# Performance work log

Measured on AMD Instinct MI355X. Metric: run time of the kernel, lower is better.

The kernel has to match this reference:

```python
import jax, jax.numpy as jnp
import numpy as np

N, K, F = 262144, 256, 128
LAMB = 1.0
EPS = 1e-16


def setup_inputs() -> dict:
    key = jax.random.key(0)
    kx, = jax.random.split(key, 1)
    x = jax.random.normal(kx, (N, F), dtype=jnp.float32)
    # Faithful SVD-orthonormal init of cluster centers (num_clusters > feature_size branch)
    rng = np.random.RandomState(0)
    m_np = rng.rand(K, F)
    m_np = m_np.T                      # (F, K) since K > F
    _, _, vh = np.linalg.svd(m_np, full_matrices=False)  # vh: (F, K)
    m_np = vh[:K].T                    # (K, F), orthonormal columns
    m = jnp.asarray(m_np, dtype=jnp.float32)
    s1 = jnp.ones((K,), dtype=jnp.float32)
    s2 = jnp.ones((K,), dtype=jnp.float32)
    return {"x": x, "m": m, "s1": s1, "s2": s2}


def _p_all(x, m, s):
    # x: (N,F), m: (K,F), s: (K,) -> p: (N,K)
    # squared distances via gram expansion (single GEMM instead of per-sample loop)
    d2 = (jnp.sum(x * x, axis=1, keepdims=True)
          + jnp.sum(m * m, axis=1)[None, :]
          - 2.0 * (x @ m.T))
    d2 = jnp.maximum(d2, 0.0)
    logits = -d2 / (s * s)[None, :]
    return jax.nn.softmax(logits, axis=-1)


def _entropy(p):
    # shannon entropy with the original's clamping of p into (0,1)
    p = jnp.clip(p, EPS, 1.0 - EPS)
    return -jnp.sum(p * jnp.log(p), axis=-1)


def reference(x, m, s1, s2):
    # F.normalize(x): L2-normalize rows with eps=1e-12
    xn = x / jnp.maximum(jnp.linalg.norm(x, axis=1, keepdims=True), 1e-12)
    p = _p_all(xn, m, s1)              # (N,K)
    intra = jnp.mean(_entropy(p))      # scalar
    # inter: entropy of the assignment of the mean center against all centers
    xm = jnp.mean(m, axis=0)           # (F,)
    d = jnp.linalg.norm(xm[None, :] - m, axis=1)  # (K,)
    pi = jax.nn.softmax(-((d / s2) ** 2))
    inter = _entropy(pi)
    total = intra - LAMB * inter
    return (total, intra, inter)
```

## Files before the change

kernel.cpp:

```cpp
#include <hip/hip_runtime.h>
#include <hip/hip_bf16.h>


#define N_ROWS 262144

typedef __attribute__((ext_vector_type(8))) short bf16x8;
typedef __attribute__((ext_vector_type(4))) float f32x4;
typedef __attribute__((ext_vector_type(4))) unsigned short u16x4;

__device__ __forceinline__ unsigned short bf16_rne(float x) {
    unsigned int u = __float_as_uint(x);
    u += 0x7FFFu + ((u >> 16) & 1u);
    return (unsigned short)(u >> 16);
}
__device__ __forceinline__ float bf16f(unsigned short h) {
    return __uint_as_float(((unsigned int)h) << 16);
}

__global__ __launch_bounds__(256) void prep(
    const float* __restrict__ m, const float* __restrict__ s1,
    unsigned short* __restrict__ mhi_g, float* __restrict__ mn2_g,
    float* __restrict__ invs_g)
{
    const int t    = threadIdx.x;
    const int lane = t & 63;
    const int k    = blockIdx.x * 8 + (t >> 5);
    const int f4   = t & 31;
    float4 v = reinterpret_cast<const float4*>(m)[k * 32 + f4];
    float pn = v.x*v.x + v.y*v.y + v.z*v.z + v.w*v.w;
    #pragma unroll
    for (int msk = 1; msk <= 16; msk <<= 1) pn += __shfl_xor(pn, msk);
    if ((lane & 31) == 0) {
        mn2_g[k] = pn;
        float sv = s1[k];
        invs_g[k] = 1.0f / (sv * sv);
    }
    const int f0 = f4 << 2;
    const int c = k >> 4, n = k & 15, s = f0 >> 5, blk = (f0 >> 3) & 3, i0 = f0 & 7;
    const int elem = ((c * 4 + s) * 64 + blk * 16 + n) * 8 + i0;
    float xs[4] = {v.x, v.y, v.z, v.w};
    u16x4 hh;
    #pragma unroll
    for (int q = 0; q < 4; ++q) hh[q] = bf16_rne(xs[q]);
    *(u16x4*)(mhi_g + elem) = hh;
}

__global__ __launch_bounds__(256, 1) void fused_main(
    const float* __restrict__ x, const unsigned short* __restrict__ mhi_g,
    const float* __restrict__ mn2_g, const float* __restrict__ invs_g,
    float* __restrict__ wavesum)
{
    const int tid  = threadIdx.x;
    const int lane = tid & 63;
    const int w    = tid >> 6;
    const int rw   = lane & 15;
    const int blkl = lane >> 4;
    const int gw   = blockIdx.x * 4 + w;

    bf16x8 B[64];
    #pragma unroll
    for (int j = 0; j < 64; ++j)
        B[j] = *(const bf16x8*)(mhi_g + (j * 64 + lane) * 8);

    float bkv[16], isv[16];
    #pragma unroll
    for (int c = 0; c < 16; ++c) {
        bkv[c] = 1.0f + mn2_g[c * 16 + rw];
        isv[c] = invs_g[c * 16 + rw];
    }

    const float* xbase = x + (size_t)(gw * 256 + rw) * 128 + blkl * 8;

    float4 px[8];
    #pragma unroll
    for (int s = 0; s < 4; ++s) {
        px[2*s]   = *(const float4*)(xbase + s * 32);
        px[2*s+1] = *(const float4*)(xbase + s * 32 + 4);
    }

    float ent = 0.0f;

    for (int t = 0; t < 16; ++t) {
        bf16x8 ah[4], al[4];
        float n2 = 0.0f;
        #pragma unroll
        for (int s = 0; s < 4; ++s) {
            float xs[8] = {px[2*s].x, px[2*s].y, px[2*s].z, px[2*s].w,
                           px[2*s+1].x, px[2*s+1].y, px[2*s+1].z, px[2*s+1].w};
            #pragma unroll
            for (int q = 0; q < 8; ++q) {
                n2 += xs[q] * xs[q];
                unsigned short h = bf16_rne(xs[q]);
                float r = xs[q] - bf16f(h);
                ah[s][q] = (short)h;
                al[s][q] = (short)bf16_rne(r);
            }
        }
        if (t != 15) {
            const float* p = xbase + (size_t)(t + 1) * 16 * 128;
            #pragma unroll
            for (int s = 0; s < 4; ++s) {
                px[2*s]   = *(const float4*)(p + s * 32);
                px[2*s+1] = *(const float4*)(p + s * 32 + 4);
            }
        }
        f32x4 acc[16];
        #pragma unroll
        for (int c = 0; c < 16; ++c) acc[c] = f32x4{0.f, 0.f, 0.f, 0.f};
        #pragma unroll
        for (int s = 0; s < 4; ++s) {
            #pragma unroll
            for (int c = 0; c < 16; ++c) {
                acc[c] = __builtin_amdgcn_mfma_f32_16x16x32_bf16(al[s], B[c*4+s], acc[c], 0, 0, 0);
                acc[c] = __builtin_amdgcn_mfma_f32_16x16x32_bf16(ah[s], B[c*4+s], acc[c], 0, 0, 0);
            }
        }
        n2 += __shfl_xor(n2, 16);
        n2 += __shfl_xor(n2, 32);
        float a2 = 2.0f / fmaxf(sqrtf(n2), 1e-12f);
        #pragma unroll
        for (int reg = 0; reg < 4; ++reg) {
            float ar = __shfl(a2, blkl * 4 + reg);
            float S = 0.f, T = 0.f;
            #pragma unroll
            for (int c = 0; c < 16; ++c) {
                float l = fminf(ar * acc[c][reg] - bkv[c], 0.0f) * isv[c];
                float e = __expf(l);
                S += e;
                T += l * e;
            }
            #pragma unroll
            for (int msk = 1; msk <= 8; msk <<= 1) {
                S += __shfl_xor(S, msk);
                T += __shfl_xor(T, msk);
            }
            if (rw == 0) ent += __logf(S) - T / S;
        }
    }

    ent += __shfl_xor(ent, 16);
    ent += __shfl_xor(ent, 32);
    if (lane == 0) wavesum[gw] = ent;
}

__global__ __launch_bounds__(1024) void finalize(
    const float* __restrict__ wavesum, const float* __restrict__ m,
    const float* __restrict__ s2, float* __restrict__ out)
{
    __shared__ float xmp[8][128];
    __shared__ float xm[128];
    __shared__ double dred[16];
    __shared__ float redS[16], redT[16];
    const int tid  = threadIdx.x;
    const int lane = tid & 63;
    const int w    = tid >> 6;

    double ds = (double)wavesum[tid];
    #pragma unroll
    for (int msk = 1; msk <= 32; msk <<= 1) ds += __shfl_xor(ds, msk);
    if (lane == 0) dred[w] = ds;

    {
        const int f = tid & 127, g = tid >> 7;
        const float* mp = m + (size_t)g * 32 * 128 + f;
        float cs = 0.f;
        #pragma unroll 8
        for (int k = 0; k < 32; ++k) cs += mp[(size_t)k * 128];
        xmp[g][f] = cs;
    }
    __syncthreads();
    if (tid < 128) {
        float s = 0.f;
        #pragma unroll
        for (int g = 0; g < 8; ++g) s += xmp[g][tid];
        xm[tid] = s * (1.0f / 256.0f);
    }
    __syncthreads();

    const int k = tid >> 2, q = tid & 3;
    float d2 = 0.f;
    {
        const float4* mr  = (const float4*)(m + (size_t)k * 128) + q * 8;
        const float4* xv4 = (const float4*)xm + q * 8;
        #pragma unroll
        for (int j = 0; j < 8; ++j) {
            float4 mv = mr[j], xv = xv4[j];
            float dx = xv.x - mv.x, dy = xv.y - mv.y,
                  dz = xv.z - mv.z, dw = xv.w - mv.w;
            d2 += dx*dx + dy*dy + dz*dz + dw*dw;
        }
    }
    d2 += __shfl_xor(d2, 1);
    d2 += __shfl_xor(d2, 2);
    float sv = s2[k];
    float rr = sqrtf(d2) / sv;
    float lg = -(rr * rr);
    float e  = (q == 0) ? __expf(lg) : 0.f;
    float S = e, T = (q == 0) ? lg * e : 0.f;
    #pragma unroll
    for (int msk = 1; msk <= 32; msk <<= 1) {
        S += __shfl_xor(S, msk);
        T += __shfl_xor(T, msk);
    }
    if (lane == 0) { redS[w] = S; redT[w] = T; }
    __syncthreads();
    if (tid == 0) {
        float Sa = 0.f, Ta = 0.f;
        double intra_d = 0.0;
        #pragma unroll
        for (int i = 0; i < 16; ++i) {
            Sa += redS[i]; Ta += redT[i]; intra_d += dred[i];
        }
        float inter = __logf(Sa) - Ta / Sa;
        float intra = (float)(intra_d / (double)N_ROWS);
        out[0] = intra - inter;
        out[1] = intra;
        out[2] = inter;
    }
}

extern "C" void kernel_launch(void* const* d_in, const int* in_sizes, int n_in,
                              void* d_out, int out_size, void* d_ws, size_t ws_size,
                              hipStream_t stream) {
    const float* x  = (const float*)d_in[0];
    const float* m  = (const float*)d_in[1];
    const float* s1 = (const float*)d_in[2];
    const float* s2 = (const float*)d_in[3];
    float* out = (float*)d_out;

    char* ws = (char*)d_ws;
    unsigned short* mhi_g = (unsigned short*)ws;
    float* mn2_g   = (float*)(ws + 65536);
    float* invs_g  = (float*)(ws + 65536 + 1024);
    float* wavesum = (float*)(ws + 65536 + 2048);

    prep<<<dim3(32), dim3(256), 0, stream>>>(m, s1, mhi_g, mn2_g, invs_g);
    fused_main<<<dim3(256), dim3(256), 0, stream>>>(x, mhi_g, mn2_g, invs_g, wavesum);
    finalize<<<dim3(1), dim3(1024), 0, stream>>>(wavesum, m, s2, out);
}
```

Baseline: 249.0 us.

## Split cluster columns across two waves per row tile and reduce softmax partials in LDS

Each 128-thread block now handles 256 rows with two waves, each wave owning half of the 256 cluster columns. This halves the B-fragment registers per wave and allows two blocks per CU. Per-row softmax partial sums (S, T) are combined through shared memory before the entropy is computed, and the grid grows to 1024 blocks. The x loads are split into two halves interleaved with the MFMA steps, and the bf16 hi/lo split uses packed conversion intrinsics. The cost is that each row's x tile is loaded and converted twice (once per wave), plus extra LDS traffic and barriers.

```diff
diff --git a/kernel.cpp b/kernel.cpp
--- a/kernel.cpp
+++ b/kernel.cpp
@@ -7,14 +7,12 @@
 typedef __attribute__((ext_vector_type(8))) short bf16x8;
 typedef __attribute__((ext_vector_type(4))) float f32x4;
 typedef __attribute__((ext_vector_type(4))) unsigned short u16x4;
+typedef __attribute__((ext_vector_type(4))) unsigned int u32x4;
 
 __device__ __forceinline__ unsigned short bf16_rne(float x) {
     unsigned int u = __float_as_uint(x);
     u += 0x7FFFu + ((u >> 16) & 1u);
     return (unsigned short)(u >> 16);
-}
-__device__ __forceinline__ float bf16f(unsigned short h) {
-    return __uint_as_float(((unsigned int)h) << 16);
 }
 
 __global__ __launch_bounds__(256) void prep(
@@ -45,102 +43,153 @@
     *(u16x4*)(mhi_g + elem) = hh;
 }
 
-__global__ __launch_bounds__(256, 1) void fused_main(
+__device__ __forceinline__ void cvt8(float4 a, float4 b, bf16x8& hi, bf16x8& lo,
+                                     float& n2a, float& n2b) {
+    float xs[8] = {a.x, a.y, a.z, a.w, b.x, b.y, b.z, b.w};
+    u32x4 hp, lp;
+    #pragma unroll
+    for (int p = 0; p < 4; ++p) {
+        float e = xs[2*p], o = xs[2*p+1];
+        n2a += e * e;
+        n2b += o * o;
+        __hip_bfloat162 hv = __float22bfloat162_rn(make_float2(e, o));
+        unsigned hu = *reinterpret_cast<unsigned*>(&hv);
+        float ef = __uint_as_float(hu << 16);
+        float of = __uint_as_float(hu & 0xffff0000u);
+        __hip_bfloat162 lv = __float22bfloat162_rn(make_float2(e - ef, o - of));
+        hp[p] = hu;
+        lp[p] = *reinterpret_cast<unsigned*>(&lv);
+    }
+    hi = *reinterpret_cast<bf16x8*>(&hp);
+    lo = *reinterpret_cast<bf16x8*>(&lp);
+}
+
+__global__ __launch_bounds__(128, 2) void fused_main(
     const float* __restrict__ x, const unsigned short* __restrict__ mhi_g,
     const float* __restrict__ mn2_g, const float* __restrict__ invs_g,
     float* __restrict__ wavesum)
 {
+    __shared__ float part[2][16][16][2];
+    __shared__ float redw[2];
+
     const int tid  = threadIdx.x;
     const int lane = tid & 63;
     const int w    = tid >> 6;
     const int rw   = lane & 15;
     const int blkl = lane >> 4;
-    const int gw   = blockIdx.x * 4 + w;
-
-    bf16x8 B[64];
-    #pragma unroll
-    for (int j = 0; j < 64; ++j)
-        B[j] = *(const bf16x8*)(mhi_g + (j * 64 + lane) * 8);
-
-    float bkv[16], isv[16];
-    #pragma unroll
-    for (int c = 0; c < 16; ++c) {
-        bkv[c] = 1.0f + mn2_g[c * 16 + rw];
-        isv[c] = invs_g[c * 16 + rw];
-    }
-
-    const float* xbase = x + (size_t)(gw * 256 + rw) * 128 + blkl * 8;
-
-    float4 px[8];
-    #pragma unroll
-    for (int s = 0; s < 4; ++s) {
-        px[2*s]   = *(const float4*)(xbase + s * 32);
-        px[2*s+1] = *(const float4*)(xbase + s * 32 + 4);
-    }
-
-    float ent = 0.0f;
+
+    bf16x8 B[32];
+    #pragma unroll
+    for (int jc = 0; jc < 8; ++jc)
+        #pragma unroll
+        for (int s = 0; s < 4; ++s)
+            B[jc*4+s] = *(const bf16x8*)(mhi_g + (((8*w + jc)*4 + s)*64 + lane)*8);
+
+    float bkv[8], isv[8];
+    #pragma unroll
+    for (int jc = 0; jc < 8; ++jc) {
+        int col = (8*w + jc)*16 + rw;
+        bkv[jc] = 1.0f + mn2_g[col];
+        isv[jc] = invs_g[col];
+    }
+
+    const float* xb = x + (size_t)(blockIdx.x*256 + rw)*128 + blkl*8;
+
+    float4 pxA[4], pxB[4];
+    #pragma unroll
+    for (int s = 0; s < 2; ++s) {
+        pxA[2*s]   = *(const float4*)(xb + s*32);
+        pxA[2*s+1] = *(const float4*)(xb + s*32 + 4);
+    }
+    #pragma unroll
+    for (int s = 2; s < 4; ++s) {
+        pxB[2*(s-2)]   = *(const float4*)(xb + s*32);
+        pxB[2*(s-2)+1] = *(const float4*)(xb + s*32 + 4);
+    }
+
+    #define MFMA_STEP(s_)                                                        \
+        do { _Pragma("unroll")                                                   \
+            for (int jc = 0; jc < 8; ++jc) {                                     \
+                acc[jc] = __builtin_amdgcn_mfma_f32_16x16x32_bf16(al, B[jc*4+(s_)], acc[jc], 0, 0, 0); \
+                acc[jc] = __builtin_amdgcn_mfma_f32_16x16x32_bf16(ah, B[jc*4+(s_)], acc[jc], 0, 0, 0); \
+            } } while (0)
 
     for (int t = 0; t < 16; ++t) {
-        bf16x8 ah[4], al[4];
-        float n2 = 0.0f;
-        #pragma unroll
-        for (int s = 0; s < 4; ++s) {
-            float xs[8] = {px[2*s].x, px[2*s].y, px[2*s].z, px[2*s].w,
-                           px[2*s+1].x, px[2*s+1].y, px[2*s+1].z, px[2*s+1].w};
-            #pragma unroll
-            for (int q = 0; q < 8; ++q) {
-                n2 += xs[q] * xs[q];
-                unsigned short h = bf16_rne(xs[q]);
-                float r = xs[q] - bf16f(h);
-                ah[s][q] = (short)h;
-                al[s][q] = (short)bf16_rne(r);
-            }
-        }
-        if (t != 15) {
-            const float* p = xbase + (size_t)(t + 1) * 16 * 128;
-            #pragma unroll
-            for (int s = 0; s < 4; ++s) {
-                px[2*s]   = *(const float4*)(p + s * 32);
-                px[2*s+1] = *(const float4*)(p + s * 32 + 4);
-            }
-        }
-        f32x4 acc[16];
-        #pragma unroll
-        for (int c = 0; c < 16; ++c) acc[c] = f32x4{0.f, 0.f, 0.f, 0.f};
-        #pragma unroll
-        for (int s = 0; s < 4; ++s) {
-            #pragma unroll
-            for (int c = 0; c < 16; ++c) {
-                acc[c] = __builtin_amdgcn_mfma_f32_16x16x32_bf16(al[s], B[c*4+s], acc[c], 0, 0, 0);
-                acc[c] = __builtin_amdgcn_mfma_f32_16x16x32_bf16(ah[s], B[c*4+s], acc[c], 0, 0, 0);
-            }
-        }
+        const float* xn = xb + (size_t)(t + 1)*2048;
+        f32x4 acc[8];
+        #pragma unroll
+        for (int jc = 0; jc < 8; ++jc) acc[jc] = f32x4{0.f, 0.f, 0.f, 0.f};
+
+        float n2a = 0.f, n2b = 0.f;
+        bf16x8 ah, al;
+
+        cvt8(pxA[0], pxA[1], ah, al, n2a, n2b);
+        MFMA_STEP(0);
+        cvt8(pxA[2], pxA[3], ah, al, n2a, n2b);
+        MFMA_STEP(1);
+        if (t < 15) {
+            #pragma unroll
+            for (int s = 0; s < 2; ++s) {
+                pxA[2*s]   = *(const float4*)(xn + s*32);
+                pxA[2*s+1] = *(const float4*)(xn + s*32 + 4);
+            }
+        }
+        cvt8(pxB[0], pxB[1], ah, al, n2a, n2b);
+        MFMA_STEP(2);
+        cvt8(pxB[2], pxB[3], ah, al, n2a, n2b);
+        MFMA_STEP(3);
+        if (t < 15) {
+            #pragma unroll
+            for (int s = 2; s < 4; ++s) {
+                pxB[2*(s-2)]   = *(const float4*)(xn + s*32);
+                pxB[2*(s-2)+1] = *(const float4*)(xn + s*32 + 4);
+            }
+        }
+
+        float n2 = n2a + n2b;
         n2 += __shfl_xor(n2, 16);
         n2 += __shfl_xor(n2, 32);
         float a2 = 2.0f / fmaxf(sqrtf(n2), 1e-12f);
         #pragma unroll
         for (int reg = 0; reg < 4; ++reg) {
-            float ar = __shfl(a2, blkl * 4 + reg);
-            float S = 0.f, T = 0.f;
-            #pragma unroll
-            for (int c = 0; c < 16; ++c) {
-                float l = fminf(ar * acc[c][reg] - bkv[c], 0.0f) * isv[c];
+            float ar = __shfl(a2, blkl*4 + reg);
+            float S0 = 0.f, S1 = 0.f, T0 = 0.f, T1 = 0.f;
+            #pragma unroll
+            for (int jc = 0; jc < 8; ++jc) {
+                float l = fminf(ar * acc[jc][reg] - bkv[jc], 0.0f) * isv[jc];
                 float e = __expf(l);
-                S += e;
-                T += l * e;
-            }
+                if (jc & 1) { S1 += e; T1 += l * e; }
+                else        { S0 += e; T0 += l * e; }
+            }
+            float S = S0 + S1, T = T0 + T1;
             #pragma unroll
             for (int msk = 1; msk <= 8; msk <<= 1) {
                 S += __shfl_xor(S, msk);
                 T += __shfl_xor(T, msk);
             }
-            if (rw == 0) ent += __logf(S) - T / S;
-        }
-    }
-
-    ent += __shfl_xor(ent, 16);
-    ent += __shfl_xor(ent, 32);
-    if (lane == 0) wavesum[gw] = ent;
+            if (rw == 0) {
+                float2 st = make_float2(S, T);
+                *(float2*)&part[w][t][blkl*4 + reg][0] = st;
+            }
+        }
+    }
+    #undef MFMA_STEP
+
+    __syncthreads();
+
+    float entloc = 0.f;
+    #pragma unroll
+    for (int r2 = 0; r2 < 2; ++r2) {
+        int r = tid*2 + r2, c = r >> 4, r16 = r & 15;
+        float S = part[0][c][r16][0] + part[1][c][r16][0];
+        float T = part[0][c][r16][1] + part[1][c][r16][1];
+        entloc += __logf(S) - T / S;
+    }
+    #pragma unroll
+    for (int msk = 1; msk <= 32; msk <<= 1) entloc += __shfl_xor(entloc, msk);
+    if (lane == 0) redw[w] = entloc;
+    __syncthreads();
+    if (tid == 0) wavesum[blockIdx.x] = redw[0] + redw[1];
 }
 
 __global__ __launch_bounds__(1024) void finalize(
@@ -235,6 +284,6 @@
     float* wavesum = (float*)(ws + 65536 + 2048);
 
     prep<<<dim3(32), dim3(256), 0, stream>>>(m, s1, mhi_g, mn2_g, invs_g);
-    fused_main<<<dim3(256), dim3(256), 0, stream>>>(x, mhi_g, mn2_g, invs_g, wavesum);
+    fused_main<<<dim3(1024), dim3(128), 0, stream>>>(x, mhi_g, mn2_g, invs_g, wavesum);
     finalize<<<dim3(1), dim3(1024), 0, stream>>>(wavesum, m, s2, out);
 }
```

New measurement: 239.4 us. 3.9% less time.

## Split cluster dimension across waves, shrink register footprint, raise occupancy

Applied to the files above, without the earlier changes.

Work is redistributed so each wave of a block holds only 64 of the 256 cluster columns in registers (16 B fragments instead of 64), and partial softmax sums are combined across waves through shared memory. The grid grows from 256 to 2048 blocks with launch bounds allowing 3 blocks per CU, aiming to hide memory latency through occupancy rather than one block per CU. The 1/s² scale and center norms are folded into the bf16 center matrix and a single per-cluster bias in prep, and x conversion uses packed bf16x2 conversions with a three-slot register prefetch ring. This adds an extra block-level reduction, shared-memory traffic and bf16 rounding of the pre-scaled centers.

```diff
diff --git a/kernel.cpp b/kernel.cpp
--- a/kernel.cpp
+++ b/kernel.cpp
@@ -13,14 +13,31 @@
     u += 0x7FFFu + ((u >> 16) & 1u);
     return (unsigned short)(u >> 16);
 }
-__device__ __forceinline__ float bf16f(unsigned short h) {
-    return __uint_as_float(((unsigned int)h) << 16);
+
+__device__ __forceinline__ void cvt8(float4 a, float4 b, bf16x8& hi, bf16x8& lo,
+                                     float& n2) {
+    float xs[8] = {a.x, a.y, a.z, a.w, b.x, b.y, b.z, b.w};
+    unsigned hp[4], lp[4];
+    #pragma unroll
+    for (int p = 0; p < 4; ++p) {
+        float e = xs[2*p], o = xs[2*p+1];
+        n2 = __builtin_fmaf(e, e, n2);
+        n2 = __builtin_fmaf(o, o, n2);
+        __hip_bfloat162 hv = __float22bfloat162_rn(make_float2(e, o));
+        unsigned hu = *reinterpret_cast<unsigned*>(&hv);
+        float ef = __uint_as_float(hu << 16);
+        float of = __uint_as_float(hu & 0xffff0000u);
+        __hip_bfloat162 lv = __float22bfloat162_rn(make_float2(e - ef, o - of));
+        hp[p] = hu;
+        lp[p] = *reinterpret_cast<unsigned*>(&lv);
+    }
+    hi = *reinterpret_cast<bf16x8*>(hp);
+    lo = *reinterpret_cast<bf16x8*>(lp);
 }
 
 __global__ __launch_bounds__(256) void prep(
     const float* __restrict__ m, const float* __restrict__ s1,
-    unsigned short* __restrict__ mhi_g, float* __restrict__ mn2_g,
-    float* __restrict__ invs_g)
+    unsigned short* __restrict__ mhi_g, float* __restrict__ p2_g)
 {
     const int t    = threadIdx.x;
     const int lane = t & 63;
@@ -30,121 +47,124 @@
     float pn = v.x*v.x + v.y*v.y + v.z*v.z + v.w*v.w;
     #pragma unroll
     for (int msk = 1; msk <= 16; msk <<= 1) pn += __shfl_xor(pn, msk);
-    if ((lane & 31) == 0) {
-        mn2_g[k] = pn;
-        float sv = s1[k];
-        invs_g[k] = 1.0f / (sv * sv);
-    }
+    float sv  = s1[k];
+    float isv = 1.0f / (sv * sv);
+    if ((lane & 31) == 0) p2_g[k] = (1.0f + pn) * isv;
     const int f0 = f4 << 2;
     const int c = k >> 4, n = k & 15, s = f0 >> 5, blk = (f0 >> 3) & 3, i0 = f0 & 7;
     const int elem = ((c * 4 + s) * 64 + blk * 16 + n) * 8 + i0;
-    float xs[4] = {v.x, v.y, v.z, v.w};
+    float xs[4] = {v.x * isv, v.y * isv, v.z * isv, v.w * isv};
     u16x4 hh;
     #pragma unroll
     for (int q = 0; q < 4; ++q) hh[q] = bf16_rne(xs[q]);
     *(u16x4*)(mhi_g + elem) = hh;
 }
 
-__global__ __launch_bounds__(256, 1) void fused_main(
+__global__ __launch_bounds__(256, 3) void fused_main(
     const float* __restrict__ x, const unsigned short* __restrict__ mhi_g,
-    const float* __restrict__ mn2_g, const float* __restrict__ invs_g,
-    float* __restrict__ wavesum)
+    const float* __restrict__ p2_g, float* __restrict__ blocksum)
 {
+    __shared__ float p2s[256];
+    __shared__ float part[8][16][4][2];
+    __shared__ float entred[4];
+
     const int tid  = threadIdx.x;
     const int lane = tid & 63;
     const int w    = tid >> 6;
     const int rw   = lane & 15;
     const int blkl = lane >> 4;
-    const int gw   = blockIdx.x * 4 + w;
-
-    bf16x8 B[64];
-    #pragma unroll
-    for (int j = 0; j < 64; ++j)
-        B[j] = *(const bf16x8*)(mhi_g + (j * 64 + lane) * 8);
-
-    float bkv[16], isv[16];
-    #pragma unroll
-    for (int c = 0; c < 16; ++c) {
-        bkv[c] = 1.0f + mn2_g[c * 16 + rw];
-        isv[c] = invs_g[c * 16 + rw];
-    }
-
-    const float* xbase = x + (size_t)(gw * 256 + rw) * 128 + blkl * 8;
-
-    float4 px[8];
-    #pragma unroll
-    for (int s = 0; s < 4; ++s) {
-        px[2*s]   = *(const float4*)(xbase + s * 32);
-        px[2*s+1] = *(const float4*)(xbase + s * 32 + 4);
-    }
-
-    float ent = 0.0f;
-
-    for (int t = 0; t < 16; ++t) {
-        bf16x8 ah[4], al[4];
-        float n2 = 0.0f;
-        #pragma unroll
-        for (int s = 0; s < 4; ++s) {
-            float xs[8] = {px[2*s].x, px[2*s].y, px[2*s].z, px[2*s].w,
-                           px[2*s+1].x, px[2*s+1].y, px[2*s+1].z, px[2*s+1].w};
+
+    p2s[tid] = p2_g[tid];
+
+    bf16x8 MB[16];
+    #pragma unroll
+    for (int tt = 0; tt < 4; ++tt)
+        #pragma unroll
+        for (int s = 0; s < 4; ++s)
+            MB[tt*4+s] = *(const bf16x8*)(mhi_g + (((4*w + tt)*4 + s)*64 + lane)*8);
+
+    __syncthreads();
+
+    const float* xb = x + (size_t)(blockIdx.x * 128 + rw) * 128 + blkl * 8;
+
+    float4 PA[3], PB[3];
+    #pragma unroll
+    for (int g = 0; g < 3; ++g) {
+        PA[g] = *(const float4*)(xb + g * 32);
+        PB[g] = *(const float4*)(xb + g * 32 + 4);
+    }
+
+    f32x4 acc[4];
+    float n2 = 0.0f;
+
+    #pragma unroll
+    for (int g = 0; g < 32; ++g) {
+        const int s = g & 3;
+        const int slot = g % 3;
+        if (s == 0) {
             #pragma unroll
-            for (int q = 0; q < 8; ++q) {
-                n2 += xs[q] * xs[q];
-                unsigned short h = bf16_rne(xs[q]);
-                float r = xs[q] - bf16f(h);
-                ah[s][q] = (short)h;
-                al[s][q] = (short)bf16_rne(r);
-            }
-        }
-        if (t != 15) {
-            const float* p = xbase + (size_t)(t + 1) * 16 * 128;
-            #pragma unroll
-            for (int s = 0; s < 4; ++s) {
-                px[2*s]   = *(const float4*)(p + s * 32);
-                px[2*s+1] = *(const float4*)(p + s * 32 + 4);
-            }
-        }
-        f32x4 acc[16];
-        #pragma unroll
-        for (int c = 0; c < 16; ++c) acc[c] = f32x4{0.f, 0.f, 0.f, 0.f};
-        #pragma unroll
-        for (int s = 0; s < 4; ++s) {
-            #pragma unroll
-            for (int c = 0; c < 16; ++c) {
-                acc[c] = __builtin_amdgcn_mfma_f32_16x16x32_bf16(al[s], B[c*4+s], acc[c], 0, 0, 0);
-                acc[c] = __builtin_amdgcn_mfma_f32_16x16x32_bf16(ah[s], B[c*4+s], acc[c], 0, 0, 0);
-            }
-        }
-        n2 += __shfl_xor(n2, 16);
-        n2 += __shfl_xor(n2, 32);
-        float a2 = 2.0f / fmaxf(sqrtf(n2), 1e-12f);
-        #pragma unroll
-        for (int reg = 0; reg < 4; ++reg) {
-            float ar = __shfl(a2, blkl * 4 + reg);
+            for (int tt = 0; tt < 4; ++tt) acc[tt] = f32x4{0.f, 0.f, 0.f, 0.f};
+            n2 = 0.0f;
+        }
+        bf16x8 ah, al;
+        cvt8(PA[slot], PB[slot], ah, al, n2);
+        if (g + 3 < 32) {
+            const int g2 = g + 3;
+            const float* p = xb + (size_t)(g2 >> 2) * 2048 + (g2 & 3) * 32;
+            PA[slot] = *(const float4*)(p);
+            PB[slot] = *(const float4*)(p + 4);
+        }
+        #pragma unroll
+        for (int tt = 0; tt < 4; ++tt) {
+            acc[tt] = __builtin_amdgcn_mfma_f32_16x16x32_bf16(MB[tt*4+s], al, acc[tt], 0, 0, 0);
+            acc[tt] = __builtin_amdgcn_mfma_f32_16x16x32_bf16(MB[tt*4+s], ah, acc[tt], 0, 0, 0);
+        }
+        if (s == 3) {
+            const int t = g >> 2;
+            float nn = n2;
+            nn += __shfl_xor(nn, 16);
+            nn += __shfl_xor(nn, 32);
+            float ar = 2.0f / fmaxf(sqrtf(nn), 1e-12f);
             float S = 0.f, T = 0.f;
             #pragma unroll
-            for (int c = 0; c < 16; ++c) {
-                float l = fminf(ar * acc[c][reg] - bkv[c], 0.0f) * isv[c];
-                float e = __expf(l);
-                S += e;
-                T += l * e;
+            for (int tt = 0; tt < 4; ++tt) {
+                f32x4 p2v = *(const f32x4*)&p2s[(4*w + tt)*16 + blkl*4];
+                #pragma unroll
+                for (int r = 0; r < 4; ++r) {
+                    float l = fminf(__builtin_fmaf(ar, acc[tt][r], -p2v[r]), 0.0f);
+                    float e = __expf(l);
+                    S += e;
+                    T = __builtin_fmaf(l, e, T);
+                }
             }
-            #pragma unroll
-            for (int msk = 1; msk <= 8; msk <<= 1) {
-                S += __shfl_xor(S, msk);
-                T += __shfl_xor(T, msk);
-            }
-            if (rw == 0) ent += __logf(S) - T / S;
-        }
-    }
-
-    ent += __shfl_xor(ent, 16);
-    ent += __shfl_xor(ent, 32);
-    if (lane == 0) wavesum[gw] = ent;
+            S += __shfl_xor(S, 16);  T += __shfl_xor(T, 16);
+            S += __shfl_xor(S, 32);  T += __shfl_xor(T, 32);
+            if (blkl == 0)
+                *(float2*)&part[t][rw][w][0] = make_float2(S, T);
+        }
+    }
+
+    __syncthreads();
+
+    float entl = 0.0f;
+    if (tid < 128) {
+        const int c = tid >> 4, r16 = tid & 15;
+        float S = part[c][r16][0][0] + part[c][r16][1][0]
+                + part[c][r16][2][0] + part[c][r16][3][0];
+        float T = part[c][r16][0][1] + part[c][r16][1][1]
+                + part[c][r16][2][1] + part[c][r16][3][1];
+        entl = __logf(S) - T / S;
+    }
+    #pragma unroll
+    for (int msk = 1; msk <= 32; msk <<= 1) entl += __shfl_xor(entl, msk);
+    if (lane == 0) entred[w] = entl;
+    __syncthreads();
+    if (tid == 0)
+        blocksum[blockIdx.x] = entred[0] + entred[1] + entred[2] + entred[3];
 }
 
 __global__ __launch_bounds__(1024) void finalize(
-    const float* __restrict__ wavesum, const float* __restrict__ m,
+    const float* __restrict__ blocksum, const float* __restrict__ m,
     const float* __restrict__ s2, float* __restrict__ out)
 {
     __shared__ float xmp[8][128];
@@ -155,7 +175,7 @@
     const int lane = tid & 63;
     const int w    = tid >> 6;
 
-    double ds = (double)wavesum[tid];
+    double ds = (double)blocksum[tid] + (double)blocksum[tid + 1024];
     #pragma unroll
     for (int msk = 1; msk <= 32; msk <<= 1) ds += __shfl_xor(ds, msk);
     if (lane == 0) dred[w] = ds;
@@ -230,11 +250,10 @@
 
     char* ws = (char*)d_ws;
     unsigned short* mhi_g = (unsigned short*)ws;
-    float* mn2_g   = (float*)(ws + 65536);
-    float* invs_g  = (float*)(ws + 65536 + 1024);
-    float* wavesum = (float*)(ws + 65536 + 2048);
-
-    prep<<<dim3(32), dim3(256), 0, stream>>>(m, s1, mhi_g, mn2_g, invs_g);
-    fused_main<<<dim3(256), dim3(256), 0, stream>>>(x, mhi_g, mn2_g, invs_g, wavesum);
-    finalize<<<dim3(1), dim3(1024), 0, stream>>>(wavesum, m, s2, out);
-}
+    float* p2_g     = (float*)(ws + 65536);
+    float* blocksum = (float*)(ws + 65536 + 1024);
+
+    prep<<<dim3(32), dim3(256), 0, stream>>>(m, s1, mhi_g, p2_g);
+    fused_main<<<dim3(2048), dim3(256), 0, stream>>>(x, mhi_g, p2_g, blocksum);
+    finalize<<<dim3(1), dim3(1024), 0, stream>>>(blocksum, m, s2, out);
+}
```

Result: faster. 231.7 us (-7.0%).
